# Kernel optimization log

Measured on AMD Instinct MI355X. Metric: run time of the kernel, lower is better.

## Reference

```python
import jax, jax.numpy as jnp
import numpy as np

N_NODES = 50000
N_EDGES = 800000
D = 64
B = 64
HL = 128  # lstm hidden
OUT = 32


def setup_inputs() -> dict:
    key = jax.random.key(0)
    ks = jax.random.split(key, 16)
    s = 0.05
    return {
        "x": jax.random.normal(ks[0], (N_NODES, D), jnp.float32),
        "edge_index": jax.random.randint(ks[1], (2, N_EDGES), 0, N_NODES),
        "batch": jnp.sort(jax.random.randint(ks[2], (N_NODES,), 0, B)),
        "w1": jax.random.normal(ks[3], (D, D), jnp.float32) * s,
        "b1": jnp.zeros((D,), jnp.float32),
        "w2": jax.random.normal(ks[4], (D, D), jnp.float32) * s,
        "b2": jnp.zeros((D,), jnp.float32),
        "w3": jax.random.normal(ks[5], (D, D), jnp.float32) * s,
        "b3": jnp.zeros((D,), jnp.float32),
        "w4": jax.random.normal(ks[6], (D, D), jnp.float32) * s,
        "b4": jnp.zeros((D,), jnp.float32),
        "w_ih": jax.random.normal(ks[7], (4 * HL, D), jnp.float32) * s,
        "w_hh": jax.random.normal(ks[8], (4 * HL, HL), jnp.float32) * s,
        "b_ih": jnp.zeros((4 * HL,), jnp.float32),
        "b_hh": jnp.zeros((4 * HL,), jnp.float32),
        "fc_w": jax.random.normal(ks[9], (OUT, HL), jnp.float32) * s,
        "fc_b": jnp.zeros((OUT,), jnp.float32),
        "h0": jax.random.normal(ks[10], (1, B, HL), jnp.float32),
        "c0": jax.random.normal(ks[11], (1, B, HL), jnp.float32),
    }


def _gin(x, edge_index, wA, bA, wB, bB):
    # GINConv with eps=0: MLP(x + sum_{j->i} x_j); scatter-add over edges
    agg = jax.ops.segment_sum(x[edge_index[0]], edge_index[1], num_segments=N_NODES)
    h = x + agg
    h = jax.nn.relu(h @ wA.T + bA)
    return h @ wB.T + bB


def reference(x, edge_index, batch, w1, b1, w2, b2, w3, b3, w4, b4,
              w_ih, w_hh, b_ih, b_hh, fc_w, fc_b, h0, c0):
    h = jax.nn.relu(_gin(x, edge_index, w1, b1, w2, b2))  # dropout = identity (eval)
    h = jax.nn.relu(_gin(h, edge_index, w3, b3, w4, b4))
    # global_mean_pool over graphs
    sums = jax.ops.segment_sum(h, batch, num_segments=B)              # [B, D]
    cnts = jax.ops.segment_sum(jnp.ones((N_NODES,), h.dtype), batch, num_segments=B)
    pooled = sums / jnp.maximum(cnts, 1.0)[:, None]
    # single-step LSTM (PyTorch gate order: i, f, g, o)
    gates = pooled @ w_ih.T + b_ih + h0[0] @ w_hh.T + b_hh            # [B, 4H]
    i, f, g, o = jnp.split(gates, 4, axis=-1)
    c1 = jax.nn.sigmoid(f) * c0[0] + jax.nn.sigmoid(i) * jnp.tanh(g)
    h1 = jax.nn.sigmoid(o) * jnp.tanh(c1)
    logits = h1 @ fc_w.T + fc_b
    probs = jax.nn.softmax(logits, axis=1)
    return probs, h1[None], c1[None]
```

## Files before the change

### kernel.cpp

```cpp
#include <hip/hip_runtime.h>
#include <hip/hip_bf16.h>

#define N_NODES 50000
#define N_EDGES 800000
#define D 64
#define B 64
#define HL 128
#define OUT 32

#define CAP 64
#define STP 72
#define ZROW N_NODES

#define BINS 196
#define EPB 2048
#define LCAP 48
#define BCAP 4608

#define AB 391
#define CB 3125

typedef __attribute__((ext_vector_type(8))) short          short8;
typedef __attribute__((ext_vector_type(8))) unsigned short ushort8_t;
typedef __attribute__((ext_vector_type(4))) float          floatx4;

__device__ __forceinline__ unsigned short f2bf(float f)
{
    unsigned u = __float_as_uint(f);
    u = (u + 0x7FFFu + ((u >> 16) & 1u)) >> 16;
    return (unsigned short)u;
}
__device__ __forceinline__ float bf2f(unsigned short s)
{
    return __uint_as_float(((unsigned)s) << 16);
}
__device__ __forceinline__ float bfLO(unsigned u) { return __uint_as_float(u << 16); }
__device__ __forceinline__ float bfHI(unsigned u) { return __uint_as_float(u & 0xffff0000u); }

__global__ __launch_bounds__(256) void fused_pro_kernel(
    const int*   __restrict__ ei,
    int*         __restrict__ bincnt,
    unsigned*    __restrict__ binbuf,
    const float* __restrict__ x, unsigned short* __restrict__ xb,
    const float* __restrict__ w1, const float* __restrict__ w2,
    const float* __restrict__ w3, const float* __restrict__ w4,
    unsigned short* __restrict__ wb,
    unsigned short* __restrict__ h1,
    float*       __restrict__ psum)
{
    __shared__ int      lcnt[BINS];
    __shared__ int      gbase[BINS];
    __shared__ unsigned lbuf[BINS * LCAP];

    int t = threadIdx.x;

    if (blockIdx.x < AB) {
        if (t < BINS) lcnt[t] = 0;
        __syncthreads();

        int base = blockIdx.x * EPB;
#pragma unroll
        for (int i = 0; i < EPB / 256; ++i) {
            int e = base + i * 256 + t;
            if (e < N_EDGES) {
                int s = ei[e];
                int d = ei[N_EDGES + e];
                int bin = d >> 8;
                unsigned pk = (unsigned)s | ((unsigned)(d & 255) << 16);
                int p = atomicAdd(&lcnt[bin], 1);
                if (p < LCAP) {
                    lbuf[bin * LCAP + p] = pk;
                } else {
                    int q = atomicAdd(&bincnt[bin], 1);
                    if (q < BCAP) binbuf[bin * BCAP + q] = pk;
                }
            }
        }
        __syncthreads();

        if (t < BINS) {
            int m = lcnt[t]; m = (m < LCAP) ? m : LCAP;
            gbase[t] = (m > 0) ? atomicAdd(&bincnt[t], m) : 0;
        }
        __syncthreads();

        int wv = t >> 6, lane = t & 63;
        for (int b = wv; b < BINS; b += 4) {
            int m = lcnt[b]; m = (m < LCAP) ? m : LCAP;
            int gb = gbase[b];
            for (int j = lane; j < m; j += 64)
                if (gb + j < BCAP) binbuf[b * BCAP + gb + j] = lbuf[b * LCAP + j];
        }
    } else if (blockIdx.x < AB + CB) {
        int cb = blockIdx.x - AB;
        int i = cb * 256 + t;
        const float4 v = reinterpret_cast<const float4*>(x)[i];
        ushort4 o;
        o.x = f2bf(v.x); o.y = f2bf(v.y); o.z = f2bf(v.z); o.w = f2bf(v.w);
        reinterpret_cast<ushort4*>(xb)[i] = o;

        if (cb < 64) {
            int j = cb * 256 + t;
            int m = j >> 12, off = j & 4095;
            const float* src = (m == 0) ? w1 : (m == 1) ? w2 : (m == 2) ? w3 : w4;
            wb[j] = f2bf(src[off]);
        }
    } else {
        if (t < D) {
            xb[(size_t)ZROW * D + t] = 0;
            h1[(size_t)ZROW * D + t] = 0;
        }
#pragma unroll
        for (int k = 0; k < 16; ++k)
            psum[t * 16 + k] = 0.0f;
    }
}

__global__ __launch_bounds__(256) void binB_kernel(
    const int*      __restrict__ bincnt,
    const unsigned* __restrict__ binbuf,
    int*            __restrict__ cnt,
    unsigned short* __restrict__ bucket)
{
    __shared__ int            lc[256];
    __shared__ unsigned short lbkt[256 * CAP];

    int t = threadIdx.x;
    lc[t] = 0;
    {
        ushort8_t fill = {ZROW, ZROW, ZROW, ZROW, ZROW, ZROW, ZROW, ZROW};
        for (int idx = t; idx < 256 * CAP / 8; idx += 256)
            reinterpret_cast<ushort8_t*>(lbkt)[idx] = fill;
    }
    __syncthreads();

    int bin = blockIdx.x;
    int m = bincnt[bin]; m = (m < BCAP) ? m : BCAP;
    const unsigned* src = binbuf + bin * BCAP;
    for (int j = t; j < m; j += 256) {
        unsigned pk = src[j];
        int dlow = (pk >> 16) & 255;
        int p = atomicAdd(&lc[dlow], 1);
        if (p < CAP) lbkt[dlow * CAP + p] = (unsigned short)(pk & 0xFFFFu);
    }
    __syncthreads();

    int n0 = bin * 256;
    int n = n0 + t;
    if (n < N_NODES) cnt[n] = (lc[t] < CAP) ? lc[t] : CAP;

    for (int idx = t; idx < 256 * 8; idx += 256) {
        int r = idx >> 3, c = idx & 7;
        if (n0 + r < N_NODES)
            *reinterpret_cast<ushort8_t*>(
                bucket + (size_t)(n0 + r) * CAP + c * 8) =
                *reinterpret_cast<const ushort8_t*>(&lbkt[r * CAP + c * 8]);
    }
}

__device__ __forceinline__ void gather16(
    const unsigned short* __restrict__ feat,
    const int*            __restrict__ cnt,
    const unsigned short* __restrict__ bucket,
    unsigned short*       stw,
    int n0, int lane)
{
    const int g = lane >> 4;
    const int c = lane & 15;

#pragma unroll
    for (int b = 0; b < 4; ++b) {
        const int node = n0 + b * 4 + g;
        int deg = cnt[node];
        deg = (deg < CAP) ? deg : CAP;
        int m = (deg + 7) >> 3;
        {
            int t1 = __shfl_xor(m, 16); m = (t1 > m) ? t1 : m;
            int t2 = __shfl_xor(m, 32); m = (t2 > m) ? t2 : m;
        }

        const unsigned short* bkt = bucket + (size_t)node * CAP;

        uint2 u = *reinterpret_cast<const uint2*>(feat + (size_t)node * D + 4 * c);
        float a0 = bfLO(u.x), a1 = bfHI(u.x);
        float a2 = bfLO(u.y), a3 = bfHI(u.y);

        ushort8_t idx = *reinterpret_cast<const ushort8_t*>(bkt);
        for (int r = 0; r < m; ++r) {
            ushort8_t nxt = *reinterpret_cast<const ushort8_t*>(bkt + (r + 1) * 8);
#pragma unroll
            for (int j = 0; j < 8; ++j) {
                uint2 v = *reinterpret_cast<const uint2*>(
                    feat + (size_t)idx[j] * D + 4 * c);
                a0 += bfLO(v.x); a1 += bfHI(v.x);
                a2 += bfLO(v.y); a3 += bfHI(v.y);
            }
            idx = nxt;
        }

        uint2 o;
        o.x = (unsigned)f2bf(a0) | ((unsigned)f2bf(a1) << 16);
        o.y = (unsigned)f2bf(a2) | ((unsigned)f2bf(a3) << 16);
        *reinterpret_cast<uint2*>(stw + (b * 4 + g) * STP + 4 * c) = o;
    }
}

__global__ __launch_bounds__(256) void gmlp_kernel(
    const unsigned short* __restrict__ feat,
    const int*            __restrict__ cnt,
    const unsigned short* __restrict__ bucket,
    const unsigned short* __restrict__ wAb,
    const float*          __restrict__ bA,
    const unsigned short* __restrict__ wBb,
    const float*          __restrict__ bB,
    unsigned short*       __restrict__ outp)
{
    __shared__ __align__(16) unsigned short st[4][16 * STP];

    const int wv   = threadIdx.x >> 6;
    const int lane = threadIdx.x & 63;
    const int quad = lane >> 4;
    const int col  = lane & 15;

    const int n0 = (blockIdx.x * 4 + wv) * 16;
    if (n0 >= N_NODES) return;

    float bAl[4], bBl[4];
#pragma unroll
    for (int t = 0; t < 4; ++t) {
        bAl[t] = bA[t * 16 + col];
        bBl[t] = bB[t * 16 + col];
    }

    short8 WA[4][2], WB[4][2];
#pragma unroll
    for (int t = 0; t < 4; ++t)
#pragma unroll
        for (int k = 0; k < 2; ++k) {
            WA[t][k] = *reinterpret_cast<const short8*>(
                wAb + (t * 16 + col) * D + k * 32 + quad * 8);
            WB[t][k] = *reinterpret_cast<const short8*>(
                wBb + (t * 16 + col) * D + k * 32 + quad * 8);
        }

    unsigned short* stw = &st[wv][0];

    gather16(feat, cnt, bucket, stw, n0, lane);

    short8 A0 = *reinterpret_cast<const short8*>(stw + col * STP + 0 * 32 + quad * 8);
    short8 A1 = *reinterpret_cast<const short8*>(stw + col * STP + 1 * 32 + quad * 8);

#pragma unroll
    for (int t = 0; t < 4; ++t) {
        floatx4 c = {0.0f, 0.0f, 0.0f, 0.0f};
        c = __builtin_amdgcn_mfma_f32_16x16x32_bf16(A0, WA[t][0], c, 0, 0, 0);
        c = __builtin_amdgcn_mfma_f32_16x16x32_bf16(A1, WA[t][1], c, 0, 0, 0);
#pragma unroll
        for (int r = 0; r < 4; ++r) {
            float v = fmaxf(c[r] + bAl[t], 0.0f);
            stw[(quad * 4 + r) * STP + t * 16 + col] = f2bf(v);
        }
    }

    short8 T0 = *reinterpret_cast<const short8*>(stw + col * STP + 0 * 32 + quad * 8);
    short8 T1 = *reinterpret_cast<const short8*>(stw + col * STP + 1 * 32 + quad * 8);

#pragma unroll
    for (int t = 0; t < 4; ++t) {
        floatx4 c = {0.0f, 0.0f, 0.0f, 0.0f};
        c = __builtin_amdgcn_mfma_f32_16x16x32_bf16(T0, WB[t][0], c, 0, 0, 0);
        c = __builtin_amdgcn_mfma_f32_16x16x32_bf16(T1, WB[t][1], c, 0, 0, 0);
#pragma unroll
        for (int r = 0; r < 4; ++r) {
            float v = fmaxf(c[r] + bBl[t], 0.0f);
            outp[(size_t)(n0 + quad * 4 + r) * D + t * 16 + col] = f2bf(v);
        }
    }
}

__global__ __launch_bounds__(256) void g2mlp_pool_kernel(
    const unsigned short* __restrict__ feat,
    const int*            __restrict__ cnt,
    const unsigned short* __restrict__ bucket,
    const unsigned short* __restrict__ wAb,
    const float*          __restrict__ bA,
    const unsigned short* __restrict__ wBb,
    const float*          __restrict__ bB,
    const int*            __restrict__ batch,
    float*                __restrict__ psum)
{
    __shared__ __align__(16) unsigned short st[4][16 * STP];
    __shared__ float pt[64][D + 1];
    __shared__ int   sbatch[64];

    const int tid  = threadIdx.x;
    const int wv   = tid >> 6;
    const int lane = tid & 63;
    const int quad = lane >> 4;
    const int col  = lane & 15;

    const int bn0 = blockIdx.x * 64;
    const int n0  = bn0 + wv * 16;
    const bool active = (n0 < N_NODES);

    if (tid < 64) {
        int n = bn0 + tid;
        sbatch[tid] = (n < N_NODES) ? batch[n] : -1;
    }

    if (active) {
        float bAl[4], bBl[4];
#pragma unroll
        for (int t = 0; t < 4; ++t) {
            bAl[t] = bA[t * 16 + col];
            bBl[t] = bB[t * 16 + col];
        }

        short8 WA[4][2], WB[4][2];
#pragma unroll
        for (int t = 0; t < 4; ++t)
#pragma unroll
            for (int k = 0; k < 2; ++k) {
                WA[t][k] = *reinterpret_cast<const short8*>(
                    wAb + (t * 16 + col) * D + k * 32 + quad * 8);
                WB[t][k] = *reinterpret_cast<const short8*>(
                    wBb + (t * 16 + col) * D + k * 32 + quad * 8);
            }

        unsigned short* stw = &st[wv][0];

        gather16(feat, cnt, bucket, stw, n0, lane);

        short8 A0 = *reinterpret_cast<const short8*>(stw + col * STP + 0 * 32 + quad * 8);
        short8 A1 = *reinterpret_cast<const short8*>(stw + col * STP + 1 * 32 + quad * 8);

#pragma unroll
        for (int t = 0; t < 4; ++t) {
            floatx4 c = {0.0f, 0.0f, 0.0f, 0.0f};
            c = __builtin_amdgcn_mfma_f32_16x16x32_bf16(A0, WA[t][0], c, 0, 0, 0);
            c = __builtin_amdgcn_mfma_f32_16x16x32_bf16(A1, WA[t][1], c, 0, 0, 0);
#pragma unroll
            for (int r = 0; r < 4; ++r) {
                float v = fmaxf(c[r] + bAl[t], 0.0f);
                stw[(quad * 4 + r) * STP + t * 16 + col] = f2bf(v);
            }
        }

        short8 T0 = *reinterpret_cast<const short8*>(stw + col * STP + 0 * 32 + quad * 8);
        short8 T1 = *reinterpret_cast<const short8*>(stw + col * STP + 1 * 32 + quad * 8);

#pragma unroll
        for (int t = 0; t < 4; ++t) {
            floatx4 c = {0.0f, 0.0f, 0.0f, 0.0f};
            c = __builtin_amdgcn_mfma_f32_16x16x32_bf16(T0, WB[t][0], c, 0, 0, 0);
            c = __builtin_amdgcn_mfma_f32_16x16x32_bf16(T1, WB[t][1], c, 0, 0, 0);
#pragma unroll
            for (int r = 0; r < 4; ++r) {
                float v = fmaxf(c[r] + bBl[t], 0.0f);
                pt[wv * 16 + quad * 4 + r][t * 16 + col] = v;
            }
        }
    } else {
#pragma unroll
        for (int r = 0; r < 4; ++r)
            pt[wv * 16 + quad * 4 + r][(lane & 15) * 4 + (lane >> 4)] = 0.0f;
        for (int c = 0; c < 4; ++c)
#pragma unroll
            for (int r = 0; r < 4; ++r)
                pt[wv * 16 + quad * 4 + r][c * 16 + col] = 0.0f;
    }
    __syncthreads();

    int q = tid >> 6;
    int d = tid & 63;
    float acc = 0.0f;
    int curg = sbatch[q * 16];
#pragma unroll
    for (int r = 0; r < 16; ++r) {
        int row = q * 16 + r;
        int g = sbatch[row];
        float v = pt[row][d];
        if (g != curg) {
            if (curg >= 0) atomicAdd(&psum[curg * D + d], acc);
            acc = 0.0f;
            curg = g;
        }
        acc += v;
    }
    if (curg >= 0) atomicAdd(&psum[curg * D + d], acc);
}

__device__ __forceinline__ int lower_bound_dev(const int* a, int n, int v)
{
    int lo = 0, hi = n;
    while (lo < hi) {
        int m = (lo + hi) >> 1;
        if (a[m] < v) lo = m + 1; else hi = m;
    }
    return lo;
}

__device__ __forceinline__ float sigmoidf_(float x) { return 1.0f / (1.0f + expf(-x)); }

__global__ __launch_bounds__(512) void head_kernel(
    const float* __restrict__ psum,
    const int*   __restrict__ batch,
    const float* __restrict__ w_ih,
    const float* __restrict__ w_hh,
    const float* __restrict__ b_ih,
    const float* __restrict__ b_hh,
    const float* __restrict__ fc_w,
    const float* __restrict__ fc_b,
    const float* __restrict__ h0,
    const float* __restrict__ c0,
    float*       __restrict__ out_probs,
    float*       __restrict__ out_h1,
    float*       __restrict__ out_c1)
{
    int b = blockIdx.x;
    int j = threadIdx.x;

    __shared__ float sp[D];
    __shared__ float sh[HL];
    __shared__ float gates[4 * HL];
    __shared__ float sh1[HL];
    __shared__ float slog[OUT];

    if (j < D) {
        int start = lower_bound_dev(batch, N_NODES, b);
        int end   = lower_bound_dev(batch, N_NODES, b + 1);
        sp[j] = psum[b * D + j] / fmaxf((float)(end - start), 1.0f);
    } else if (j < D + HL) {
        sh[j - D] = h0[b * HL + (j - D)];
    }
    __syncthreads();

    {
        float acc = b_ih[j] + b_hh[j];
#pragma unroll
        for (int k = 0; k < D; ++k)  acc = fmaf(sp[k], w_ih[j * D + k], acc);
#pragma unroll
        for (int k = 0; k < HL; ++k) acc = fmaf(sh[k], w_hh[j * HL + k], acc);
        gates[j] = acc;
    }
    __syncthreads();

    if (j < HL) {
        float ig = gates[j];
        float fg = gates[HL + j];
        float gg = gates[2 * HL + j];
        float og = gates[3 * HL + j];
        float c  = sigmoidf_(fg) * c0[b * HL + j] + sigmoidf_(ig) * tanhf(gg);
        float hv = sigmoidf_(og) * tanhf(c);
        out_c1[b * HL + j] = c;
        out_h1[b * HL + j] = hv;
        sh1[j] = hv;
    }
    __syncthreads();

    if (j < OUT) {
        float a = fc_b[j];
#pragma unroll
        for (int k = 0; k < HL; ++k) a = fmaf(sh1[k], fc_w[j * HL + k], a);
        slog[j] = a;
    }
    __syncthreads();

    if (j < OUT) {
        float m = -1e30f;
#pragma unroll
        for (int k = 0; k < OUT; ++k) m = fmaxf(m, slog[k]);
        float s = 0.0f;
#pragma unroll
        for (int k = 0; k < OUT; ++k) s += expf(slog[k] - m);
        out_probs[b * OUT + j] = expf(slog[j] - m) / s;
    }
}

extern "C" void kernel_launch(void* const* d_in, const int* in_sizes, int n_in,
                              void* d_out, int out_size, void* d_ws, size_t ws_size,
                              hipStream_t stream)
{
    const float* x     = (const float*)d_in[0];
    const int*   ei    = (const int*)  d_in[1];
    const int*   batch = (const int*)  d_in[2];
    const float* w1    = (const float*)d_in[3];
    const float* b1    = (const float*)d_in[4];
    const float* w2    = (const float*)d_in[5];
    const float* b2    = (const float*)d_in[6];
    const float* w3    = (const float*)d_in[7];
    const float* b3    = (const float*)d_in[8];
    const float* w4    = (const float*)d_in[9];
    const float* b4    = (const float*)d_in[10];
    const float* w_ih  = (const float*)d_in[11];
    const float* w_hh  = (const float*)d_in[12];
    const float* b_ih  = (const float*)d_in[13];
    const float* b_hh  = (const float*)d_in[14];
    const float* fc_w  = (const float*)d_in[15];
    const float* fc_b  = (const float*)d_in[16];
    const float* h0    = (const float*)d_in[17];
    const float* c0    = (const float*)d_in[18];

    const size_t NR = (size_t)N_NODES + 16;
    int* bincnt = (int*)d_ws;
    int* cnt    = bincnt + 256;
    unsigned* binbuf = (unsigned*)(cnt + N_NODES);
    unsigned short* bucket = (unsigned short*)(binbuf + (size_t)BINS * BCAP);
    unsigned short* xb = bucket + (size_t)N_NODES * CAP;
    unsigned short* g  = xb + NR * D;
    unsigned short* h1 = g  + NR * D;
    unsigned short* wb = h1 + NR * D;
    float* psum = (float*)(wb + 4 * D * D);
    (void)g;

    float* out_probs = (float*)d_out;
    float* out_h1    = out_probs + B * OUT;
    float* out_c1    = out_h1 + B * HL;

    const int mb = (N_NODES / 16 + 3) / 4;

    hipMemsetAsync(bincnt, 0, 256 * sizeof(int), stream);
    fused_pro_kernel<<<AB + CB + 1, 256, 0, stream>>>(
        ei, bincnt, binbuf, x, xb, w1, w2, w3, w4, wb, h1, psum);

    binB_kernel<<<BINS, 256, 0, stream>>>(bincnt, binbuf, cnt, bucket);

    gmlp_kernel<<<mb, 256, 0, stream>>>(xb, cnt, bucket, wb, b1, wb + 4096, b2, h1);

    g2mlp_pool_kernel<<<mb, 256, 0, stream>>>(h1, cnt, bucket,
                                              wb + 8192, b3, wb + 12288, b4,
                                              batch, psum);

    head_kernel<<<B, 512, 0, stream>>>(psum, batch, w_ih, w_hh, b_ih, b_hh,
                                       fc_w, fc_b, h0, c0,
                                       out_probs, out_h1, out_c1);
}
```

Measured before the change: 202.2 us.

## Fuse all GNN stages into one persistent cooperative kernel with grid syncs

Replaces the five kernel launches with a single cooperative persistent kernel that loops over tiles and separates the stages (edge binning plus conversion, bucket build, first GIN MLP, second GIN MLP with pooling, LSTM head) with grid.sync(). Part of the x-to-bf16 conversion is moved into the bucket-build phase to balance work across the stages. The aim is to remove launch gaps and tail effects between the small kernels. In exchange, grid size is capped at 1024 blocks, MLP weights are reloaded in registers per phase, and grid barriers add their own cost. The old multi-kernel path remains as a fallback if the cooperative launch fails.

```diff
diff --git a/kernel.cpp b/kernel.cpp
--- a/kernel.cpp
+++ b/kernel.cpp
@@ -1,5 +1,8 @@
 #include <hip/hip_runtime.h>
 #include <hip/hip_bf16.h>
+#include <hip/hip_cooperative_groups.h>
+
+namespace cg = cooperative_groups;
 
 #define N_NODES 50000
 #define N_EDGES 800000
@@ -19,6 +22,13 @@
 
 #define AB 391
 #define CB 3125
+#define MB 782
+
+#define CVT_A 1563
+#define CVT_B (CB - CVT_A)
+
+#define NT0A (AB + CVT_A)
+#define NT0B (BINS + CVT_B + 1)
 
 typedef __attribute__((ext_vector_type(8))) short          short8;
 typedef __attribute__((ext_vector_type(8))) unsigned short ushort8_t;
@@ -36,6 +46,439 @@
 }
 __device__ __forceinline__ float bfLO(unsigned u) { return __uint_as_float(u << 16); }
 __device__ __forceinline__ float bfHI(unsigned u) { return __uint_as_float(u & 0xffff0000u); }
+
+__device__ __forceinline__ int lower_bound_dev(const int* a, int n, int v)
+{
+    int lo = 0, hi = n;
+    while (lo < hi) {
+        int m = (lo + hi) >> 1;
+        if (a[m] < v) lo = m + 1; else hi = m;
+    }
+    return lo;
+}
+
+__device__ __forceinline__ float sigmoidf_(float x) { return 1.0f / (1.0f + expf(-x)); }
+
+__device__ __forceinline__ void gather16(
+    const unsigned short* __restrict__ feat,
+    const int*            __restrict__ cnt,
+    const unsigned short* __restrict__ bucket,
+    unsigned short*       stw,
+    int n0, int lane)
+{
+    const int g = lane >> 4;
+    const int c = lane & 15;
+
+#pragma unroll
+    for (int b = 0; b < 4; ++b) {
+        const int node = n0 + b * 4 + g;
+        int deg = cnt[node];
+        deg = (deg < CAP) ? deg : CAP;
+        int m = (deg + 7) >> 3;
+        {
+            int t1 = __shfl_xor(m, 16); m = (t1 > m) ? t1 : m;
+            int t2 = __shfl_xor(m, 32); m = (t2 > m) ? t2 : m;
+        }
+
+        const unsigned short* bkt = bucket + (size_t)node * CAP;
+
+        uint2 u = *reinterpret_cast<const uint2*>(feat + (size_t)node * D + 4 * c);
+        float a0 = bfLO(u.x), a1 = bfHI(u.x);
+        float a2 = bfLO(u.y), a3 = bfHI(u.y);
+
+        ushort8_t idx = *reinterpret_cast<const ushort8_t*>(bkt);
+        for (int r = 0; r < m; ++r) {
+            ushort8_t nxt = *reinterpret_cast<const ushort8_t*>(bkt + (r + 1) * 8);
+#pragma unroll
+            for (int j = 0; j < 8; ++j) {
+                uint2 v = *reinterpret_cast<const uint2*>(
+                    feat + (size_t)idx[j] * D + 4 * c);
+                a0 += bfLO(v.x); a1 += bfHI(v.x);
+                a2 += bfLO(v.y); a3 += bfHI(v.y);
+            }
+            idx = nxt;
+        }
+
+        uint2 o;
+        o.x = (unsigned)f2bf(a0) | ((unsigned)f2bf(a1) << 16);
+        o.y = (unsigned)f2bf(a2) | ((unsigned)f2bf(a3) << 16);
+        *reinterpret_cast<uint2*>(stw + (b * 4 + g) * STP + 4 * c) = o;
+    }
+}
+
+__global__ __launch_bounds__(256) void onekernel(
+    const int*   __restrict__ ei,
+    int*         __restrict__ bincnt,
+    unsigned*    __restrict__ binbuf,
+    const float* __restrict__ x,
+    unsigned short* __restrict__ xb,
+    const float* __restrict__ w1, const float* __restrict__ w2,
+    const float* __restrict__ w3, const float* __restrict__ w4,
+    unsigned short* __restrict__ wb,
+    unsigned short* __restrict__ h1,
+    float*       __restrict__ psum,
+    int*         __restrict__ cnt,
+    unsigned short* __restrict__ bucket,
+    const int*   __restrict__ batch,
+    const float* __restrict__ b1, const float* __restrict__ b2,
+    const float* __restrict__ b3, const float* __restrict__ b4,
+    const float* __restrict__ w_ih, const float* __restrict__ w_hh,
+    const float* __restrict__ b_ih, const float* __restrict__ b_hh,
+    const float* __restrict__ fc_w, const float* __restrict__ fc_b,
+    const float* __restrict__ h0,  const float* __restrict__ c0,
+    float* __restrict__ out_probs,
+    float* __restrict__ out_h1,
+    float* __restrict__ out_c1)
+{
+    __shared__ __align__(16) unsigned char smem[39232];
+
+    cg::grid_group grid = cg::this_grid();
+
+    const int t    = threadIdx.x;
+    const int wv   = t >> 6;
+    const int lane = t & 63;
+    const int quad = lane >> 4;
+    const int col  = lane & 15;
+
+    {
+        int* lcnt  = (int*)smem;
+        int* gbase = lcnt + BINS;
+        unsigned* lbuf = (unsigned*)(gbase + BINS);
+
+        for (int tile = blockIdx.x; tile < NT0A; tile += gridDim.x) {
+            if (tile < AB) {
+                if (t < BINS) lcnt[t] = 0;
+                __syncthreads();
+
+                int base = tile * EPB;
+#pragma unroll
+                for (int i = 0; i < EPB / 256; ++i) {
+                    int e = base + i * 256 + t;
+                    if (e < N_EDGES) {
+                        int s = ei[e];
+                        int d = ei[N_EDGES + e];
+                        int bin = d >> 8;
+                        unsigned pk = (unsigned)s | ((unsigned)(d & 255) << 16);
+                        int p = atomicAdd(&lcnt[bin], 1);
+                        if (p < LCAP) {
+                            lbuf[bin * LCAP + p] = pk;
+                        } else {
+                            int q = atomicAdd(&bincnt[bin], 1);
+                            if (q < BCAP) binbuf[bin * BCAP + q] = pk;
+                        }
+                    }
+                }
+                __syncthreads();
+
+                if (t < BINS) {
+                    int m = lcnt[t]; m = (m < LCAP) ? m : LCAP;
+                    gbase[t] = (m > 0) ? atomicAdd(&bincnt[t], m) : 0;
+                }
+                __syncthreads();
+
+                for (int b = wv; b < BINS; b += 4) {
+                    int m = lcnt[b]; m = (m < LCAP) ? m : LCAP;
+                    int gb = gbase[b];
+                    for (int j = lane; j < m; j += 64)
+                        if (gb + j < BCAP) binbuf[b * BCAP + gb + j] = lbuf[b * LCAP + j];
+                }
+                __syncthreads();
+            } else {
+                int cb = tile - AB;
+                int i = cb * 256 + t;
+                const float4 v = reinterpret_cast<const float4*>(x)[i];
+                ushort4 o;
+                o.x = f2bf(v.x); o.y = f2bf(v.y); o.z = f2bf(v.z); o.w = f2bf(v.w);
+                reinterpret_cast<ushort4*>(xb)[i] = o;
+
+                if (cb < 64) {
+                    int j = cb * 256 + t;
+                    int m = j >> 12, off = j & 4095;
+                    const float* src = (m == 0) ? w1 : (m == 1) ? w2 : (m == 2) ? w3 : w4;
+                    wb[j] = f2bf(src[off]);
+                }
+            }
+        }
+    }
+    grid.sync();
+
+    {
+        int* lc = (int*)smem;
+        unsigned short* lbkt = (unsigned short*)(smem + 1024);
+
+        for (int tile = blockIdx.x; tile < NT0B; tile += gridDim.x) {
+            if (tile < BINS) {
+                lc[t] = 0;
+                {
+                    ushort8_t fill = {ZROW, ZROW, ZROW, ZROW, ZROW, ZROW, ZROW, ZROW};
+                    for (int idx = t; idx < 256 * CAP / 8; idx += 256)
+                        reinterpret_cast<ushort8_t*>(lbkt)[idx] = fill;
+                }
+                __syncthreads();
+
+                int bin = tile;
+                int m = bincnt[bin]; m = (m < BCAP) ? m : BCAP;
+                const unsigned* src = binbuf + bin * BCAP;
+                for (int j = t; j < m; j += 256) {
+                    unsigned pk = src[j];
+                    int dlow = (pk >> 16) & 255;
+                    int p = atomicAdd(&lc[dlow], 1);
+                    if (p < CAP) lbkt[dlow * CAP + p] = (unsigned short)(pk & 0xFFFFu);
+                }
+                __syncthreads();
+
+                int n0b = bin * 256;
+                int n = n0b + t;
+                if (n < N_NODES) cnt[n] = (lc[t] < CAP) ? lc[t] : CAP;
+
+                for (int idx = t; idx < 256 * 8; idx += 256) {
+                    int r = idx >> 3, c2 = idx & 7;
+                    if (n0b + r < N_NODES)
+                        *reinterpret_cast<ushort8_t*>(
+                            bucket + (size_t)(n0b + r) * CAP + c2 * 8) =
+                            *reinterpret_cast<const ushort8_t*>(&lbkt[r * CAP + c2 * 8]);
+                }
+                __syncthreads();
+            } else if (tile < BINS + CVT_B) {
+                int cb = CVT_A + (tile - BINS);
+                int i = cb * 256 + t;
+                const float4 v = reinterpret_cast<const float4*>(x)[i];
+                ushort4 o;
+                o.x = f2bf(v.x); o.y = f2bf(v.y); o.z = f2bf(v.z); o.w = f2bf(v.w);
+                reinterpret_cast<ushort4*>(xb)[i] = o;
+            } else {
+                if (t < D) {
+                    xb[(size_t)ZROW * D + t] = 0;
+                    h1[(size_t)ZROW * D + t] = 0;
+                }
+#pragma unroll
+                for (int k = 0; k < 16; ++k)
+                    psum[t * 16 + k] = 0.0f;
+            }
+        }
+    }
+    grid.sync();
+
+    {
+        unsigned short* stw = (unsigned short*)smem + wv * (16 * STP);
+        const unsigned short* wAb = wb;
+        const unsigned short* wBb = wb + 4096;
+
+        float bAl[4], bBl[4];
+#pragma unroll
+        for (int tt = 0; tt < 4; ++tt) {
+            bAl[tt] = b1[tt * 16 + col];
+            bBl[tt] = b2[tt * 16 + col];
+        }
+        short8 WA[4][2], WB[4][2];
+#pragma unroll
+        for (int tt = 0; tt < 4; ++tt)
+#pragma unroll
+            for (int k = 0; k < 2; ++k) {
+                WA[tt][k] = *reinterpret_cast<const short8*>(
+                    wAb + (tt * 16 + col) * D + k * 32 + quad * 8);
+                WB[tt][k] = *reinterpret_cast<const short8*>(
+                    wBb + (tt * 16 + col) * D + k * 32 + quad * 8);
+            }
+
+        for (int tile = blockIdx.x; tile < MB; tile += gridDim.x) {
+            const int n0 = (tile * 4 + wv) * 16;
+            if (n0 < N_NODES) {
+                gather16(xb, cnt, bucket, stw, n0, lane);
+
+                short8 A0 = *reinterpret_cast<const short8*>(stw + col * STP + 0 * 32 + quad * 8);
+                short8 A1 = *reinterpret_cast<const short8*>(stw + col * STP + 1 * 32 + quad * 8);
+
+#pragma unroll
+                for (int tt = 0; tt < 4; ++tt) {
+                    floatx4 c = {0.0f, 0.0f, 0.0f, 0.0f};
+                    c = __builtin_amdgcn_mfma_f32_16x16x32_bf16(A0, WA[tt][0], c, 0, 0, 0);
+                    c = __builtin_amdgcn_mfma_f32_16x16x32_bf16(A1, WA[tt][1], c, 0, 0, 0);
+#pragma unroll
+                    for (int r = 0; r < 4; ++r) {
+                        float v = fmaxf(c[r] + bAl[tt], 0.0f);
+                        stw[(quad * 4 + r) * STP + tt * 16 + col] = f2bf(v);
+                    }
+                }
+
+                short8 T0 = *reinterpret_cast<const short8*>(stw + col * STP + 0 * 32 + quad * 8);
+                short8 T1 = *reinterpret_cast<const short8*>(stw + col * STP + 1 * 32 + quad * 8);
+
+#pragma unroll
+                for (int tt = 0; tt < 4; ++tt) {
+                    floatx4 c = {0.0f, 0.0f, 0.0f, 0.0f};
+                    c = __builtin_amdgcn_mfma_f32_16x16x32_bf16(T0, WB[tt][0], c, 0, 0, 0);
+                    c = __builtin_amdgcn_mfma_f32_16x16x32_bf16(T1, WB[tt][1], c, 0, 0, 0);
+#pragma unroll
+                    for (int r = 0; r < 4; ++r) {
+                        float v = fmaxf(c[r] + bBl[tt], 0.0f);
+                        h1[(size_t)(n0 + quad * 4 + r) * D + tt * 16 + col] = f2bf(v);
+                    }
+                }
+            }
+        }
+    }
+    grid.sync();
+
+    {
+        unsigned short* stw = (unsigned short*)smem + wv * (16 * STP);
+        float (*pt)[D + 1] = (float (*)[D + 1])(smem + 9216);
+        int* sbatch = (int*)(smem + 9216 + 16640);
+        const unsigned short* wAb = wb + 8192;
+        const unsigned short* wBb = wb + 12288;
+
+        float bAl[4], bBl[4];
+#pragma unroll
+        for (int tt = 0; tt < 4; ++tt) {
+            bAl[tt] = b3[tt * 16 + col];
+            bBl[tt] = b4[tt * 16 + col];
+        }
+        short8 WA[4][2], WB[4][2];
+#pragma unroll
+        for (int tt = 0; tt < 4; ++tt)
+#pragma unroll
+            for (int k = 0; k < 2; ++k) {
+                WA[tt][k] = *reinterpret_cast<const short8*>(
+                    wAb + (tt * 16 + col) * D + k * 32 + quad * 8);
+                WB[tt][k] = *reinterpret_cast<const short8*>(
+                    wBb + (tt * 16 + col) * D + k * 32 + quad * 8);
+            }
+
+        for (int tile = blockIdx.x; tile < MB; tile += gridDim.x) {
+            const int bn0 = tile * 64;
+            const int n0  = bn0 + wv * 16;
+            const bool active = (n0 < N_NODES);
+
+            if (t < 64) {
+                int n = bn0 + t;
+                sbatch[t] = (n < N_NODES) ? batch[n] : -1;
+            }
+
+            if (active) {
+                gather16(h1, cnt, bucket, stw, n0, lane);
+
+                short8 A0 = *reinterpret_cast<const short8*>(stw + col * STP + 0 * 32 + quad * 8);
+                short8 A1 = *reinterpret_cast<const short8*>(stw + col * STP + 1 * 32 + quad * 8);
+
+#pragma unroll
+                for (int tt = 0; tt < 4; ++tt) {
+                    floatx4 c = {0.0f, 0.0f, 0.0f, 0.0f};
+                    c = __builtin_amdgcn_mfma_f32_16x16x32_bf16(A0, WA[tt][0], c, 0, 0, 0);
+                    c = __builtin_amdgcn_mfma_f32_16x16x32_bf16(A1, WA[tt][1], c, 0, 0, 0);
+#pragma unroll
+                    for (int r = 0; r < 4; ++r) {
+                        float v = fmaxf(c[r] + bAl[tt], 0.0f);
+                        stw[(quad * 4 + r) * STP + tt * 16 + col] = f2bf(v);
+                    }
+                }
+
+                short8 T0 = *reinterpret_cast<const short8*>(stw + col * STP + 0 * 32 + quad * 8);
+                short8 T1 = *reinterpret_cast<const short8*>(stw + col * STP + 1 * 32 + quad * 8);
+
+#pragma unroll
+                for (int tt = 0; tt < 4; ++tt) {
+                    floatx4 c = {0.0f, 0.0f, 0.0f, 0.0f};
+                    c = __builtin_amdgcn_mfma_f32_16x16x32_bf16(T0, WB[tt][0], c, 0, 0, 0);
+                    c = __builtin_amdgcn_mfma_f32_16x16x32_bf16(T1, WB[tt][1], c, 0, 0, 0);
+#pragma unroll
+                    for (int r = 0; r < 4; ++r) {
+                        float v = fmaxf(c[r] + bBl[tt], 0.0f);
+                        pt[wv * 16 + quad * 4 + r][tt * 16 + col] = v;
+                    }
+                }
+            } else {
+                for (int c2 = 0; c2 < 4; ++c2)
+#pragma unroll
+                    for (int r = 0; r < 4; ++r)
+                        pt[wv * 16 + quad * 4 + r][c2 * 16 + col] = 0.0f;
+            }
+            __syncthreads();
+
+            {
+                int q = t >> 6;
+                int d = t & 63;
+                float acc = 0.0f;
+                int curg = sbatch[q * 16];
+#pragma unroll
+                for (int r = 0; r < 16; ++r) {
+                    int row = q * 16 + r;
+                    int g2 = sbatch[row];
+                    float v = pt[row][d];
+                    if (g2 != curg) {
+                        if (curg >= 0) atomicAdd(&psum[curg * D + d], acc);
+                        acc = 0.0f;
+                        curg = g2;
+                    }
+                    acc += v;
+                }
+                if (curg >= 0) atomicAdd(&psum[curg * D + d], acc);
+            }
+            __syncthreads();
+        }
+    }
+    grid.sync();
+
+    if (blockIdx.x < B) {
+        float* sp    = (float*)smem;
+        float* sh    = sp + D;
+        float* gates = sh + HL;
+        float* sh1   = gates + 4 * HL;
+        float* slog  = sh1 + HL;
+
+        int b = blockIdx.x;
+        int j = t;
+
+        if (j < D) {
+            int start = lower_bound_dev(batch, N_NODES, b);
+            int end   = lower_bound_dev(batch, N_NODES, b + 1);
+            sp[j] = psum[b * D + j] / fmaxf((float)(end - start), 1.0f);
+        } else if (j < D + HL) {
+            sh[j - D] = h0[b * HL + (j - D)];
+        }
+        __syncthreads();
+
+        for (int jj = j; jj < 4 * HL; jj += 256) {
+            float acc = b_ih[jj] + b_hh[jj];
+#pragma unroll
+            for (int k = 0; k < D; ++k)  acc = fmaf(sp[k], w_ih[jj * D + k], acc);
+#pragma unroll
+            for (int k = 0; k < HL; ++k) acc = fmaf(sh[k], w_hh[jj * HL + k], acc);
+            gates[jj] = acc;
+        }
+        __syncthreads();
+
+        if (j < HL) {
+            float ig = gates[j];
+            float fg = gates[HL + j];
+            float gg = gates[2 * HL + j];
+            float og = gates[3 * HL + j];
+            float c  = sigmoidf_(fg) * c0[b * HL + j] + sigmoidf_(ig) * tanhf(gg);
+            float hv = sigmoidf_(og) * tanhf(c);
+            out_c1[b * HL + j] = c;
+            out_h1[b * HL + j] = hv;
+            sh1[j] = hv;
+        }
+        __syncthreads();
+
+        if (j < OUT) {
+            float a = fc_b[j];
+#pragma unroll
+            for (int k = 0; k < HL; ++k) a = fmaf(sh1[k], fc_w[j * HL + k], a);
+            slog[j] = a;
+        }
+        __syncthreads();
+
+        if (j < OUT) {
+            float m = -1e30f;
+#pragma unroll
+            for (int k = 0; k < OUT; ++k) m = fmaxf(m, slog[k]);
+            float s = 0.0f;
+#pragma unroll
+            for (int k = 0; k < OUT; ++k) s += expf(slog[k] - m);
+            out_probs[b * OUT + j] = expf(slog[j] - m) / s;
+        }
+    }
+}
 
 __global__ __launch_bounds__(256) void fused_pro_kernel(
     const int*   __restrict__ ei,
@@ -158,53 +601,6 @@
     }
 }
 
-__device__ __forceinline__ void gather16(
-    const unsigned short* __restrict__ feat,
-    const int*            __restrict__ cnt,
-    const unsigned short* __restrict__ bucket,
-    unsigned short*       stw,
-    int n0, int lane)
-{
-    const int g = lane >> 4;
-    const int c = lane & 15;
-
-#pragma unroll
-    for (int b = 0; b < 4; ++b) {
-        const int node = n0 + b * 4 + g;
-        int deg = cnt[node];
-        deg = (deg < CAP) ? deg : CAP;
-        int m = (deg + 7) >> 3;
-        {
-            int t1 = __shfl_xor(m, 16); m = (t1 > m) ? t1 : m;
-            int t2 = __shfl_xor(m, 32); m = (t2 > m) ? t2 : m;
-        }
-
-        const unsigned short* bkt = bucket + (size_t)node * CAP;
-
-        uint2 u = *reinterpret_cast<const uint2*>(feat + (size_t)node * D + 4 * c);
-        float a0 = bfLO(u.x), a1 = bfHI(u.x);
-        float a2 = bfLO(u.y), a3 = bfHI(u.y);
-
-        ushort8_t idx = *reinterpret_cast<const ushort8_t*>(bkt);
-        for (int r = 0; r < m; ++r) {
-            ushort8_t nxt = *reinterpret_cast<const ushort8_t*>(bkt + (r + 1) * 8);
-#pragma unroll
-            for (int j = 0; j < 8; ++j) {
-                uint2 v = *reinterpret_cast<const uint2*>(
-                    feat + (size_t)idx[j] * D + 4 * c);
-                a0 += bfLO(v.x); a1 += bfHI(v.x);
-                a2 += bfLO(v.y); a3 += bfHI(v.y);
-            }
-            idx = nxt;
-        }
-
-        uint2 o;
-        o.x = (unsigned)f2bf(a0) | ((unsigned)f2bf(a1) << 16);
-        o.y = (unsigned)f2bf(a2) | ((unsigned)f2bf(a3) << 16);
-        *reinterpret_cast<uint2*>(stw + (b * 4 + g) * STP + 4 * c) = o;
-    }
-}
-
 __global__ __launch_bounds__(256) void gmlp_kernel(
     const unsigned short* __restrict__ feat,
     const int*            __restrict__ cnt,
@@ -361,9 +757,6 @@
             }
         }
     } else {
-#pragma unroll
-        for (int r = 0; r < 4; ++r)
-            pt[wv * 16 + quad * 4 + r][(lane & 15) * 4 + (lane >> 4)] = 0.0f;
         for (int c = 0; c < 4; ++c)
 #pragma unroll
             for (int r = 0; r < 4; ++r)
@@ -389,18 +782,6 @@
     }
     if (curg >= 0) atomicAdd(&psum[curg * D + d], acc);
 }
-
-__device__ __forceinline__ int lower_bound_dev(const int* a, int n, int v)
-{
-    int lo = 0, hi = n;
-    while (lo < hi) {
-        int m = (lo + hi) >> 1;
-        if (a[m] < v) lo = m + 1; else hi = m;
-    }
-    return lo;
-}
-
-__device__ __forceinline__ float sigmoidf_(float x) { return 1.0f / (1.0f + expf(-x)); }
 
 __global__ __launch_bounds__(512) void head_kernel(
     const float* __restrict__ psum,
@@ -517,20 +898,66 @@
     float* out_h1    = out_probs + B * OUT;
     float* out_c1    = out_h1 + B * HL;
 
+    hipMemsetAsync(bincnt, 0, 256 * sizeof(int), stream);
+
+    static int g_blocks = 0;
+    if (g_blocks == 0) {
+        int maxB = 0;
+        hipError_t oe = hipOccupancyMaxActiveBlocksPerMultiprocessor(
+            &maxB, (const void*)onekernel, 256, 0);
+        if (oe != hipSuccess || maxB < 1) maxB = 1;
+        long gsz = (long)maxB * 256;
+        if (gsz > 1024) gsz = 1024;
+        if (gsz < 64)   gsz = 64;
+        g_blocks = (int)gsz;
+    }
+
+    {
+        const int*   ei_    = ei;
+        int*         bincnt_ = bincnt;
+        unsigned*    binbuf_ = binbuf;
+        const float* x_     = x;
+        unsigned short* xb_ = xb;
+        const float* w1_ = w1; const float* w2_ = w2;
+        const float* w3_ = w3; const float* w4_ = w4;
+        unsigned short* wb_ = wb;
+        unsigned short* h1_ = h1;
+        float*       psum_ = psum;
+        int*         cnt_  = cnt;
+        unsigned short* bucket_ = bucket;
+        const int*   batch_ = batch;
+        const float* b1_ = b1; const float* b2_ = b2;
+        const float* b3_ = b3; const float* b4_ = b4;
+        const float* wih_ = w_ih; const float* whh_ = w_hh;
+        const float* bih_ = b_ih; const float* bhh_ = b_hh;
+        const float* fcw_ = fc_w; const float* fcb_ = fc_b;
+        const float* h0_ = h0; const float* c0_ = c0;
+        float* op_ = out_probs; float* oh_ = out_h1; float* oc_ = out_c1;
+
+        void* kargs[] = {
+            (void*)&ei_, (void*)&bincnt_, (void*)&binbuf_, (void*)&x_, (void*)&xb_,
+            (void*)&w1_, (void*)&w2_, (void*)&w3_, (void*)&w4_, (void*)&wb_,
+            (void*)&h1_, (void*)&psum_, (void*)&cnt_, (void*)&bucket_, (void*)&batch_,
+            (void*)&b1_, (void*)&b2_, (void*)&b3_, (void*)&b4_,
+            (void*)&wih_, (void*)&whh_, (void*)&bih_, (void*)&bhh_,
+            (void*)&fcw_, (void*)&fcb_, (void*)&h0_, (void*)&c0_,
+            (void*)&op_, (void*)&oh_, (void*)&oc_
+        };
+
+        hipError_t err = hipLaunchCooperativeKernel(
+            (const void*)onekernel, dim3(g_blocks), dim3(256), kargs, 0, stream);
+
+        if (err == hipSuccess) return;
+    }
+
     const int mb = (N_NODES / 16 + 3) / 4;
-
-    hipMemsetAsync(bincnt, 0, 256 * sizeof(int), stream);
     fused_pro_kernel<<<AB + CB + 1, 256, 0, stream>>>(
         ei, bincnt, binbuf, x, xb, w1, w2, w3, w4, wb, h1, psum);
-
     binB_kernel<<<BINS, 256, 0, stream>>>(bincnt, binbuf, cnt, bucket);
-
     gmlp_kernel<<<mb, 256, 0, stream>>>(xb, cnt, bucket, wb, b1, wb + 4096, b2, h1);
-
     g2mlp_pool_kernel<<<mb, 256, 0, stream>>>(h1, cnt, bucket,
                                               wb + 8192, b3, wb + 12288, b4,
                                               batch, psum);
-
     head_kernel<<<B, 512, 0, stream>>>(psum, batch, w_ih, w_hh, b_ih, b_hh,
                                        fc_w, fc_b, h0, c0,
                                        out_probs, out_h1, out_c1);
```

New measurement: 394.9 us. 1.95x slower.

## Build per-node edge buckets in LDS inside the GIN MLP kernels

Applied to the files above, without the earlier changes.

Removes the separate binB kernel and its global bucket/cnt arrays. Each MLP block builds its 64 nodes' neighbor lists in shared memory straight from the coarse bin buffer, and the gather reads indices from LDS. This saves one launch and the global write and re-read of the bucket table. In exchange each block scans its whole 256-node bin (about 4K entries) and keeps only a quarter of it, and both GIN layers repeat this work, so binning traffic is roughly quadrupled and LDS use per block grows.

```diff
diff --git a/kernel.cpp b/kernel.cpp
--- a/kernel.cpp
+++ b/kernel.cpp
@@ -19,6 +19,7 @@
 
 #define AB 391
 #define CB 3125
+#define MB 782
 
 typedef __attribute__((ext_vector_type(8))) short          short8;
 typedef __attribute__((ext_vector_type(8))) unsigned short ushort8_t;
@@ -116,62 +117,52 @@
     }
 }
 
-__global__ __launch_bounds__(256) void binB_kernel(
+__device__ __forceinline__ void build_bucket64(
     const int*      __restrict__ bincnt,
     const unsigned* __restrict__ binbuf,
-    int*            __restrict__ cnt,
-    unsigned short* __restrict__ bucket)
-{
-    __shared__ int            lc[256];
-    __shared__ unsigned short lbkt[256 * CAP];
-
-    int t = threadIdx.x;
-    lc[t] = 0;
+    unsigned short* lbkt,
+    int*            lc,
+    int bn0, int t)
+{
     {
         ushort8_t fill = {ZROW, ZROW, ZROW, ZROW, ZROW, ZROW, ZROW, ZROW};
-        for (int idx = t; idx < 256 * CAP / 8; idx += 256)
-            reinterpret_cast<ushort8_t*>(lbkt)[idx] = fill;
-    }
-    __syncthreads();
-
-    int bin = blockIdx.x;
+        reinterpret_cast<ushort8_t*>(lbkt)[t]       = fill;
+        reinterpret_cast<ushort8_t*>(lbkt)[t + 256] = fill;
+    }
+    if (t < 64) lc[t] = 0;
+    __syncthreads();
+
+    const int bin = bn0 >> 8;
+    const int q   = (bn0 >> 6) & 3;
     int m = bincnt[bin]; m = (m < BCAP) ? m : BCAP;
     const unsigned* src = binbuf + bin * BCAP;
     for (int j = t; j < m; j += 256) {
         unsigned pk = src[j];
         int dlow = (pk >> 16) & 255;
-        int p = atomicAdd(&lc[dlow], 1);
-        if (p < CAP) lbkt[dlow * CAP + p] = (unsigned short)(pk & 0xFFFFu);
-    }
-    __syncthreads();
-
-    int n0 = bin * 256;
-    int n = n0 + t;
-    if (n < N_NODES) cnt[n] = (lc[t] < CAP) ? lc[t] : CAP;
-
-    for (int idx = t; idx < 256 * 8; idx += 256) {
-        int r = idx >> 3, c = idx & 7;
-        if (n0 + r < N_NODES)
-            *reinterpret_cast<ushort8_t*>(
-                bucket + (size_t)(n0 + r) * CAP + c * 8) =
-                *reinterpret_cast<const ushort8_t*>(&lbkt[r * CAP + c * 8]);
-    }
-}
-
-__device__ __forceinline__ void gather16(
+        if ((dlow >> 6) == q) {
+            int r = dlow & 63;
+            int p = atomicAdd(&lc[r], 1);
+            if (p < CAP) lbkt[r * CAP + p] = (unsigned short)(pk & 0xFFFFu);
+        }
+    }
+    __syncthreads();
+}
+
+__device__ __forceinline__ void gather16_lds(
     const unsigned short* __restrict__ feat,
-    const int*            __restrict__ cnt,
-    const unsigned short* __restrict__ bucket,
+    const unsigned short* lbkt,
+    const int*            lc,
     unsigned short*       stw,
-    int n0, int lane)
+    int bn0, int wv, int lane)
 {
     const int g = lane >> 4;
     const int c = lane & 15;
 
 #pragma unroll
     for (int b = 0; b < 4; ++b) {
-        const int node = n0 + b * 4 + g;
-        int deg = cnt[node];
+        const int rloc = wv * 16 + b * 4 + g;
+        const int node = bn0 + rloc;
+        int deg = lc[rloc];
         deg = (deg < CAP) ? deg : CAP;
         int m = (deg + 7) >> 3;
         {
@@ -179,7 +170,7 @@
             int t2 = __shfl_xor(m, 32); m = (t2 > m) ? t2 : m;
         }
 
-        const unsigned short* bkt = bucket + (size_t)node * CAP;
+        const unsigned short* bkt = lbkt + rloc * CAP;
 
         uint2 u = *reinterpret_cast<const uint2*>(feat + (size_t)node * D + 4 * c);
         float a0 = bfLO(u.x), a1 = bfHI(u.x);
@@ -207,58 +198,65 @@
 
 __global__ __launch_bounds__(256) void gmlp_kernel(
     const unsigned short* __restrict__ feat,
-    const int*            __restrict__ cnt,
-    const unsigned short* __restrict__ bucket,
+    const int*            __restrict__ bincnt,
+    const unsigned*       __restrict__ binbuf,
     const unsigned short* __restrict__ wAb,
     const float*          __restrict__ bA,
     const unsigned short* __restrict__ wBb,
     const float*          __restrict__ bB,
     unsigned short*       __restrict__ outp)
 {
+    __shared__ int lc[64];
+    __shared__ __align__(16) unsigned short lbkt[64 * CAP + 16];
     __shared__ __align__(16) unsigned short st[4][16 * STP];
 
-    const int wv   = threadIdx.x >> 6;
-    const int lane = threadIdx.x & 63;
+    const int t    = threadIdx.x;
+    const int wv   = t >> 6;
+    const int lane = t & 63;
     const int quad = lane >> 4;
     const int col  = lane & 15;
 
-    const int n0 = (blockIdx.x * 4 + wv) * 16;
+    const int bn0 = blockIdx.x * 64;
+    const int n0  = bn0 + wv * 16;
+
+    build_bucket64(bincnt, binbuf, lbkt, lc, bn0, t);
+
     if (n0 >= N_NODES) return;
 
     float bAl[4], bBl[4];
 #pragma unroll
-    for (int t = 0; t < 4; ++t) {
-        bAl[t] = bA[t * 16 + col];
-        bBl[t] = bB[t * 16 + col];
+    for (int tt = 0; tt < 4; ++tt) {
+        bAl[tt] = bA[tt * 16 + col];
+        bBl[tt] = bB[tt * 16 + col];
     }
 
     short8 WA[4][2], WB[4][2];
 #pragma unroll
-    for (int t = 0; t < 4; ++t)
+    for (int tt = 0; tt < 4; ++tt)
 #pragma unroll
         for (int k = 0; k < 2; ++k) {
-            WA[t][k] = *reinterpret_cast<const short8*>(
-                wAb + (t * 16 + col) * D + k * 32 + quad * 8);
-            WB[t][k] = *reinterpret_cast<const short8*>(
-                wBb + (t * 16 + col) * D + k * 32 + quad * 8);
+            WA[tt][k] = *reinterpret_cast<const short8*>(
+                wAb + (tt * 16 + col) * D + k * 32 + quad * 8);
+            WB[tt][k] = *reinterpret_cast<const short8*>(
+                wBb + (tt * 16 + col) * D + k * 32 + quad * 8);
         }
 
     unsigned short* stw = &st[wv][0];
 
-    gather16(feat, cnt, bucket, stw, n0, lane);
+    gather16_lds(feat, lbkt, lc, stw, bn0, wv, lane);
 
     short8 A0 = *reinterpret_cast<const short8*>(stw + col * STP + 0 * 32 + quad * 8);
     short8 A1 = *reinterpret_cast<const short8*>(stw + col * STP + 1 * 32 + quad * 8);
 
 #pragma unroll
-    for (int t = 0; t < 4; ++t) {
+    for (int tt = 0; tt < 4; ++tt) {
         floatx4 c = {0.0f, 0.0f, 0.0f, 0.0f};
-        c = __builtin_amdgcn_mfma_f32_16x16x32_bf16(A0, WA[t][0], c, 0, 0, 0);
-        c = __builtin_amdgcn_mfma_f32_16x16x32_bf16(A1, WA[t][1], c, 0, 0, 0);
+        c = __builtin_amdgcn_mfma_f32_16x16x32_bf16(A0, WA[tt][0], c, 0, 0, 0);
+        c = __builtin_amdgcn_mfma_f32_16x16x32_bf16(A1, WA[tt][1], c, 0, 0, 0);
 #pragma unroll
         for (int r = 0; r < 4; ++r) {
-            float v = fmaxf(c[r] + bAl[t], 0.0f);
-            stw[(quad * 4 + r) * STP + t * 16 + col] = f2bf(v);
+            float v = fmaxf(c[r] + bAl[tt], 0.0f);
+            stw[(quad * 4 + r) * STP + tt * 16 + col] = f2bf(v);
         }
     }
 
@@ -266,22 +264,22 @@
     short8 T1 = *reinterpret_cast<const short8*>(stw + col * STP + 1 * 32 + quad * 8);
 
 #pragma unroll
-    for (int t = 0; t < 4; ++t) {
+    for (int tt = 0; tt < 4; ++tt) {
         floatx4 c = {0.0f, 0.0f, 0.0f, 0.0f};
-        c = __builtin_amdgcn_mfma_f32_16x16x32_bf16(T0, WB[t][0], c, 0, 0, 0);
-        c = __builtin_amdgcn_mfma_f32_16x16x32_bf16(T1, WB[t][1], c, 0, 0, 0);
+        c = __builtin_amdgcn_mfma_f32_16x16x32_bf16(T0, WB[tt][0], c, 0, 0, 0);
+        c = __builtin_amdgcn_mfma_f32_16x16x32_bf16(T1, WB[tt][1], c, 0, 0, 0);
 #pragma unroll
         for (int r = 0; r < 4; ++r) {
-            float v = fmaxf(c[r] + bBl[t], 0.0f);
-            outp[(size_t)(n0 + quad * 4 + r) * D + t * 16 + col] = f2bf(v);
+            float v = fmaxf(c[r] + bBl[tt], 0.0f);
+            outp[(size_t)(n0 + quad * 4 + r) * D + tt * 16 + col] = f2bf(v);
         }
     }
 }
 
 __global__ __launch_bounds__(256) void g2mlp_pool_kernel(
     const unsigned short* __restrict__ feat,
-    const int*            __restrict__ cnt,
-    const unsigned short* __restrict__ bucket,
+    const int*            __restrict__ bincnt,
+    const unsigned*       __restrict__ binbuf,
     const unsigned short* __restrict__ wAb,
     const float*          __restrict__ bA,
     const unsigned short* __restrict__ wBb,
@@ -289,13 +287,15 @@
     const int*            __restrict__ batch,
     float*                __restrict__ psum)
 {
+    __shared__ int lc[64];
+    __shared__ __align__(16) unsigned short lbkt[64 * CAP + 16];
     __shared__ __align__(16) unsigned short st[4][16 * STP];
     __shared__ float pt[64][D + 1];
     __shared__ int   sbatch[64];
 
-    const int tid  = threadIdx.x;
-    const int wv   = tid >> 6;
-    const int lane = tid & 63;
+    const int t    = threadIdx.x;
+    const int wv   = t >> 6;
+    const int lane = t & 63;
     const int quad = lane >> 4;
     const int col  = lane & 15;
 
@@ -303,46 +303,48 @@
     const int n0  = bn0 + wv * 16;
     const bool active = (n0 < N_NODES);
 
-    if (tid < 64) {
-        int n = bn0 + tid;
-        sbatch[tid] = (n < N_NODES) ? batch[n] : -1;
-    }
+    if (t < 64) {
+        int n = bn0 + t;
+        sbatch[t] = (n < N_NODES) ? batch[n] : -1;
+    }
+
+    build_bucket64(bincnt, binbuf, lbkt, lc, bn0, t);
 
     if (active) {
         float bAl[4], bBl[4];
 #pragma unroll
-        for (int t = 0; t < 4; ++t) {
-            bAl[t] = bA[t * 16 + col];
-            bBl[t] = bB[t * 16 + col];
+        for (int tt = 0; tt < 4; ++tt) {
+            bAl[tt] = bA[tt * 16 + col];
+            bBl[tt] = bB[tt * 16 + col];
         }
 
         short8 WA[4][2], WB[4][2];
 #pragma unroll
-        for (int t = 0; t < 4; ++t)
+        for (int tt = 0; tt < 4; ++tt)
 #pragma unroll
             for (int k = 0; k < 2; ++k) {
-                WA[t][k] = *reinterpret_cast<const short8*>(
-                    wAb + (t * 16 + col) * D + k * 32 + quad * 8);
-                WB[t][k] = *reinterpret_cast<const short8*>(
-                    wBb + (t * 16 + col) * D + k * 32 + quad * 8);
+                WA[tt][k] = *reinterpret_cast<const short8*>(
+                    wAb + (tt * 16 + col) * D + k * 32 + quad * 8);
+                WB[tt][k] = *reinterpret_cast<const short8*>(
+                    wBb + (tt * 16 + col) * D + k * 32 + quad * 8);
             }
 
         unsigned short* stw = &st[wv][0];
 
-        gather16(feat, cnt, bucket, stw, n0, lane);
+        gather16_lds(feat, lbkt, lc, stw, bn0, wv, lane);
 
         short8 A0 = *reinterpret_cast<const short8*>(stw + col * STP + 0 * 32 + quad * 8);
         short8 A1 = *reinterpret_cast<const short8*>(stw + col * STP + 1 * 32 + quad * 8);
 
 #pragma unroll
-        for (int t = 0; t < 4; ++t) {
+        for (int tt = 0; tt < 4; ++tt) {
             floatx4 c = {0.0f, 0.0f, 0.0f, 0.0f};
-            c = __builtin_amdgcn_mfma_f32_16x16x32_bf16(A0, WA[t][0], c, 0, 0, 0);
-            c = __builtin_amdgcn_mfma_f32_16x16x32_bf16(A1, WA[t][1], c, 0, 0, 0);
+            c = __builtin_amdgcn_mfma_f32_16x16x32_bf16(A0, WA[tt][0], c, 0, 0, 0);
+            c = __builtin_amdgcn_mfma_f32_16x16x32_bf16(A1, WA[tt][1], c, 0, 0, 0);
 #pragma unroll
             for (int r = 0; r < 4; ++r) {
-                float v = fmaxf(c[r] + bAl[t], 0.0f);
-                stw[(quad * 4 + r) * STP + t * 16 + col] = f2bf(v);
+                float v = fmaxf(c[r] + bAl[tt], 0.0f);
+                stw[(quad * 4 + r) * STP + tt * 16 + col] = f2bf(v);
             }
         }
 
@@ -350,40 +352,37 @@
         short8 T1 = *reinterpret_cast<const short8*>(stw + col * STP + 1 * 32 + quad * 8);
 
 #pragma unroll
-        for (int t = 0; t < 4; ++t) {
+        for (int tt = 0; tt < 4; ++tt) {
             floatx4 c = {0.0f, 0.0f, 0.0f, 0.0f};
-            c = __builtin_amdgcn_mfma_f32_16x16x32_bf16(T0, WB[t][0], c, 0, 0, 0);
-            c = __builtin_amdgcn_mfma_f32_16x16x32_bf16(T1, WB[t][1], c, 0, 0, 0);
+            c = __builtin_amdgcn_mfma_f32_16x16x32_bf16(T0, WB[tt][0], c, 0, 0, 0);
+            c = __builtin_amdgcn_mfma_f32_16x16x32_bf16(T1, WB[tt][1], c, 0, 0, 0);
 #pragma unroll
             for (int r = 0; r < 4; ++r) {
-                float v = fmaxf(c[r] + bBl[t], 0.0f);
-                pt[wv * 16 + quad * 4 + r][t * 16 + col] = v;
+                float v = fmaxf(c[r] + bBl[tt], 0.0f);
+                pt[wv * 16 + quad * 4 + r][tt * 16 + col] = v;
             }
         }
     } else {
-#pragma unroll
-        for (int r = 0; r < 4; ++r)
-            pt[wv * 16 + quad * 4 + r][(lane & 15) * 4 + (lane >> 4)] = 0.0f;
-        for (int c = 0; c < 4; ++c)
+        for (int c2 = 0; c2 < 4; ++c2)
 #pragma unroll
             for (int r = 0; r < 4; ++r)
-                pt[wv * 16 + quad * 4 + r][c * 16 + col] = 0.0f;
-    }
-    __syncthreads();
-
-    int q = tid >> 6;
-    int d = tid & 63;
+                pt[wv * 16 + quad * 4 + r][c2 * 16 + col] = 0.0f;
+    }
+    __syncthreads();
+
+    int q = t >> 6;
+    int d = t & 63;
     float acc = 0.0f;
     int curg = sbatch[q * 16];
 #pragma unroll
     for (int r = 0; r < 16; ++r) {
         int row = q * 16 + r;
-        int g = sbatch[row];
+        int g2 = sbatch[row];
         float v = pt[row][d];
-        if (g != curg) {
+        if (g2 != curg) {
             if (curg >= 0) atomicAdd(&psum[curg * D + d], acc);
             acc = 0.0f;
-            curg = g;
+            curg = g2;
         }
         acc += v;
     }
@@ -503,31 +502,24 @@
 
     const size_t NR = (size_t)N_NODES + 16;
     int* bincnt = (int*)d_ws;
-    int* cnt    = bincnt + 256;
-    unsigned* binbuf = (unsigned*)(cnt + N_NODES);
-    unsigned short* bucket = (unsigned short*)(binbuf + (size_t)BINS * BCAP);
-    unsigned short* xb = bucket + (size_t)N_NODES * CAP;
-    unsigned short* g  = xb + NR * D;
-    unsigned short* h1 = g  + NR * D;
+    unsigned* binbuf = (unsigned*)(bincnt + 256);
+    unsigned short* xb = (unsigned short*)(binbuf + (size_t)BINS * BCAP);
+    unsigned short* h1 = xb + NR * D;
     unsigned short* wb = h1 + NR * D;
     float* psum = (float*)(wb + 4 * D * D);
-    (void)g;
 
     float* out_probs = (float*)d_out;
     float* out_h1    = out_probs + B * OUT;
     float* out_c1    = out_h1 + B * HL;
 
-    const int mb = (N_NODES / 16 + 3) / 4;
-
     hipMemsetAsync(bincnt, 0, 256 * sizeof(int), stream);
     fused_pro_kernel<<<AB + CB + 1, 256, 0, stream>>>(
         ei, bincnt, binbuf, x, xb, w1, w2, w3, w4, wb, h1, psum);
 
-    binB_kernel<<<BINS, 256, 0, stream>>>(bincnt, binbuf, cnt, bucket);
-
-    gmlp_kernel<<<mb, 256, 0, stream>>>(xb, cnt, bucket, wb, b1, wb + 4096, b2, h1);
-
-    g2mlp_pool_kernel<<<mb, 256, 0, stream>>>(h1, cnt, bucket,
+    gmlp_kernel<<<MB, 256, 0, stream>>>(xb, bincnt, binbuf,
+                                        wb, b1, wb + 4096, b2, h1);
+
+    g2mlp_pool_kernel<<<MB, 256, 0, stream>>>(h1, bincnt, binbuf,
                                               wb + 8192, b3, wb + 12288, b4,
                                               batch, psum);
 
```

New measurement: 199.0 us. Within noise of the previous version (-1.6%).
